# Performance work log

Measured on AMD Instinct MI355X. Metric: run time of the kernel, lower is better.

Reference implementation:

```python
import jax, jax.numpy as jnp
import numpy as np

TEMPERATURE = 0.07
EPS = 1e-8  # F.cosine_similarity eps


def setup_inputs() -> dict:
    key = jax.random.key(0)
    k1, k2, k3, k4 = jax.random.split(key, 4)
    N, D, M, C = 4096, 1024, 8192, 100
    q = jax.random.normal(k1, (N, D), dtype=jnp.float32)
    labels = jax.random.randint(k2, (N,), 0, C, dtype=jnp.int32)
    memory_logits = jax.random.normal(k3, (N, M), dtype=jnp.float32)
    memory_targets = jax.random.bernoulli(k4, 0.5, (N, M)).astype(jnp.float32)
    return {"q": q, "labels": labels, "memory_logits": memory_logits,
            "memory_targets": memory_targets}


def reference(q, labels, memory_logits, memory_targets):
    N = q.shape[0]
    # cosine similarity as normalize + GEMM (second operand detached, as in torch)
    qn = q / jnp.maximum(jnp.linalg.norm(q, axis=-1, keepdims=True), EPS)
    sims = qn @ jax.lax.stop_gradient(qn).T               # [N, N]
    src_contrast = sims / TEMPERATURE
    logits_max = jax.lax.stop_gradient(
        jnp.max(src_contrast, axis=1, keepdims=True))
    src_logits = src_contrast - logits_max                # [N, N]
    # positive-pair mask with self excluded
    src_targets = (labels[:, None] == labels[None, :]).astype(jnp.float32)
    self_mask = 1.0 - jnp.eye(N, dtype=jnp.float32)
    src_targets = src_targets * self_mask
    targets = jnp.concatenate([src_targets, memory_targets], axis=1)  # [N, N+M]
    src_exp_logits = jnp.exp(src_logits) * self_mask
    logits = jnp.concatenate([src_logits, memory_logits], axis=1)     # [N, N+M]
    denom = src_exp_logits.sum(axis=1) + jnp.exp(memory_logits).sum(axis=1)
    log_prob = logits - jnp.log(denom)[:, None]
    mean_log_prob_pos = (targets * log_prob).sum(axis=1) / targets.sum(axis=1)
    return -jnp.mean(mean_log_prob_pos)
```

## Files before the change

### kernel.cpp

```cpp
#include <hip/hip_runtime.h>
#include <hip/hip_bf16.h>
#include <math.h>

typedef unsigned short u16;
typedef __bf16 bf16x8 __attribute__((ext_vector_type(8)));
typedef float f32x4 __attribute__((ext_vector_type(4)));
typedef unsigned short u16x4 __attribute__((ext_vector_type(4)));

#define NROW 4096
#define KDIM 1024
#define MDIM 8192
#define TILE 128
#define BK 64
#define NT   (NROW / TILE)
#define NSEG (NT * 2)
#define NTRI (NT * (NT + 1) / 2)

__device__ __forceinline__ u16 f2bf(float x) {
    unsigned int u = __float_as_uint(x);
    unsigned int r = (u + 0x7fffu + ((u >> 16) & 1u)) >> 16;
    return (u16)r;
}

__device__ __forceinline__ void gload16(const u16* g, u16* l) {
    __builtin_amdgcn_global_load_lds(
        (const __attribute__((address_space(1))) void*)g,
        (__attribute__((address_space(3))) void*)l,
        16, 0, 0);
}

__global__ void k_norm_mem(const float* __restrict__ q,
                           const float* __restrict__ ml, const float* __restrict__ mt,
                           u16* __restrict__ qn, float4* __restrict__ memq) {
    const int r = blockIdx.x;
    const int t = threadIdx.x;
    const int lane = t & 63, wid = t >> 6;

    const float4* qr = (const float4*)(q + (size_t)r * KDIM);
    float4 v = qr[t];
    float ss = v.x * v.x + v.y * v.y + v.z * v.z + v.w * v.w;

    const float4* pl = (const float4*)(ml + (size_t)r * MDIM);
    const float4* pt = (const float4*)(mt + (size_t)r * MDIM);
    float S2 = 0.f, dot = 0.f, smt = 0.f;
    #pragma unroll
    for (int it = 0; it < 2; ++it) {
        const int i0 = it * 1024 + t;
        float4 l0 = pl[i0], l1 = pl[i0 + 256], l2 = pl[i0 + 512], l3 = pl[i0 + 768];
        float4 t0 = pt[i0], t1 = pt[i0 + 256], t2 = pt[i0 + 512], t3 = pt[i0 + 768];
        S2 += __expf(l0.x) + __expf(l0.y) + __expf(l0.z) + __expf(l0.w);
        S2 += __expf(l1.x) + __expf(l1.y) + __expf(l1.z) + __expf(l1.w);
        S2 += __expf(l2.x) + __expf(l2.y) + __expf(l2.z) + __expf(l2.w);
        S2 += __expf(l3.x) + __expf(l3.y) + __expf(l3.z) + __expf(l3.w);
        dot += t0.x * l0.x + t0.y * l0.y + t0.z * l0.z + t0.w * l0.w;
        dot += t1.x * l1.x + t1.y * l1.y + t1.z * l1.z + t1.w * l1.w;
        dot += t2.x * l2.x + t2.y * l2.y + t2.z * l2.z + t2.w * l2.w;
        dot += t3.x * l3.x + t3.y * l3.y + t3.z * l3.z + t3.w * l3.w;
        smt += t0.x + t0.y + t0.z + t0.w + t1.x + t1.y + t1.z + t1.w;
        smt += t2.x + t2.y + t2.z + t2.w + t3.x + t3.y + t3.z + t3.w;
    }

    #pragma unroll
    for (int d = 1; d < 64; d <<= 1) ss += __shfl_xor(ss, d);
    __shared__ float redn[4];
    if (lane == 0) redn[wid] = ss;
    __syncthreads();
    float tot = redn[0] + redn[1] + redn[2] + redn[3];
    float inv = 1.0f / fmaxf(sqrtf(tot), 1e-8f);
    u16x4 o;
    o[0] = f2bf(v.x * inv); o[1] = f2bf(v.y * inv);
    o[2] = f2bf(v.z * inv); o[3] = f2bf(v.w * inv);
    *(u16x4*)(qn + (size_t)r * KDIM + t * 4) = o;

    #pragma unroll
    for (int d = 1; d < 64; d <<= 1) {
        S2  += __shfl_xor(S2, d);
        dot += __shfl_xor(dot, d);
        smt += __shfl_xor(smt, d);
    }
    __shared__ float red[4][3];
    if (lane == 0) { red[wid][0] = S2; red[wid][1] = dot; red[wid][2] = smt; }
    __syncthreads();
    if (t == 0)
        memq[r] = make_float4(red[0][0] + red[1][0] + red[2][0] + red[3][0],
                              red[0][1] + red[1][1] + red[2][1] + red[3][1],
                              red[0][2] + red[1][2] + red[2][2] + red[3][2], 0.f);
}

__global__ void k_gemm_sym(const u16* __restrict__ qn, const int* __restrict__ labels,
                           float4* __restrict__ partials) {
    __shared__ u16 ldsA[TILE * BK];
    __shared__ u16 ldsB[TILE * BK];
    __shared__ int labR[TILE], labC[TILE];

    const int bid = blockIdx.x;
    int e = (bid & 7) * 66 + (bid >> 3);
    int rb, cb, base;
    if      (e < 36)  { rb = 0; cb = 0; base = 0;   }
    else if (e < 100) { rb = 0; cb = 1; base = 36;  }
    else if (e < 136) { rb = 1; cb = 1; base = 100; }
    else if (e < 200) { rb = 0; cb = 2; base = 136; }
    else if (e < 264) { rb = 1; cb = 2; base = 200; }
    else if (e < 300) { rb = 2; cb = 2; base = 264; }
    else if (e < 364) { rb = 0; cb = 3; base = 300; }
    else if (e < 428) { rb = 1; cb = 3; base = 364; }
    else if (e < 492) { rb = 2; cb = 3; base = 428; }
    else              { rb = 3; cb = 3; base = 492; }
    int k = e - base;
    int bi, ct;
    if (rb == cb) {
        int b2 = 0, kk = k;
        while (kk >= 8 - b2) { kk -= 8 - b2; ++b2; }
        bi = rb * 8 + b2; ct = cb * 8 + b2 + kk;
    } else {
        bi = rb * 8 + (k >> 3); ct = cb * 8 + (k & 7);
    }

    const int t = threadIdx.x;
    const int w = t >> 6, lane = t & 63;
    const int rowbase = bi * TILE, colbase = ct * TILE;

    if (t < 128) labR[t] = labels[rowbase + t];
    else labC[t - 128] = labels[colbase + (t - 128)];

    const int wr = (w >> 1) * 64, wc = (w & 1) * 64;
    const int cl = lane & 15, cg = lane >> 4;
    const int sr = lane >> 3, skb = lane & 7;

    f32x4 acc[4][4];
    #pragma unroll
    for (int i = 0; i < 4; ++i)
        #pragma unroll
        for (int j = 0; j < 4; ++j)
            acc[i][j] = {0.f, 0.f, 0.f, 0.f};

    for (int ks = 0; ks < KDIM / BK; ++ks) {
        const int k0 = ks * BK;
        #pragma unroll
        for (int it = 0; it < 4; ++it) {
            int c = w * 4 + it;
            int rr = c * 8 + sr;
            gload16(qn + (size_t)(rowbase + rr) * KDIM + k0 + skb * 8, ldsA + c * 512);
            gload16(qn + (size_t)(colbase + rr) * KDIM + k0 + skb * 8, ldsB + c * 512);
        }
        asm volatile("s_waitcnt vmcnt(0)" ::: "memory");
        __syncthreads();
        #pragma unroll
        for (int k2 = 0; k2 < 2; ++k2) {
            bf16x8 a[4], b[4];
            #pragma unroll
            for (int f = 0; f < 4; ++f) {
                a[f] = *(const bf16x8*)&ldsA[(wr + f * 16 + cl) * BK + k2 * 32 + cg * 8];
                b[f] = *(const bf16x8*)&ldsB[(wc + f * 16 + cl) * BK + k2 * 32 + cg * 8];
            }
            #pragma unroll
            for (int fm = 0; fm < 4; ++fm)
                #pragma unroll
                for (int fn = 0; fn < 4; ++fn)
                    acc[fm][fn] = __builtin_amdgcn_mfma_f32_16x16x32_bf16(
                        a[fm], b[fn], acc[fm][fn], 0, 0, 0);
        }
        __syncthreads();
    }

    const float invT = (float)(1.0 / 0.07);

    #pragma unroll
    for (int fm = 0; fm < 4; ++fm) {
        #pragma unroll
        for (int reg = 0; reg < 4; ++reg) {
            const int lr = wr + fm * 16 + cg * 4 + reg;
            const int gi = rowbase + lr;
            const int li = labR[lr];
            float c0 = acc[fm][0][reg] * invT;
            float c1 = acc[fm][1][reg] * invT;
            float c2 = acc[fm][2][reg] * invT;
            float c3 = acc[fm][3][reg] * invT;
            float m = fmaxf(fmaxf(c0, c1), fmaxf(c2, c3));
            #pragma unroll
            for (int d = 1; d < 16; d <<= 1) m = fmaxf(m, __shfl_xor(m, d));
            float se = 0.f, ps = 0.f, cnt = 0.f;
            #pragma unroll
            for (int fn = 0; fn < 4; ++fn) {
                float c = (fn == 0) ? c0 : (fn == 1) ? c1 : (fn == 2) ? c2 : c3;
                const int lc = wc + fn * 16 + cl;
                const bool self = (colbase + lc == gi);
                se += self ? 0.f : __expf(c - m);
                const bool pos = (!self) && (labC[lc] == li);
                ps += pos ? c : 0.f;
                cnt += pos ? 1.f : 0.f;
            }
            #pragma unroll
            for (int d = 1; d < 16; d <<= 1) {
                se  += __shfl_xor(se, d);
                ps  += __shfl_xor(ps, d);
                cnt += __shfl_xor(cnt, d);
            }
            if (cl == 0)
                partials[(size_t)(ct * 2 + (w & 1)) * NROW + gi] =
                    make_float4(m, se, ps, cnt);
        }
    }

    if (bi != ct) {
        #pragma unroll
        for (int fn = 0; fn < 4; ++fn) {
            const int lc = wc + fn * 16 + cl;
            const int gj = colbase + lc;
            const int lj = labC[lc];
            float m = -3.4e38f;
            #pragma unroll
            for (int fm = 0; fm < 4; ++fm)
                #pragma unroll
                for (int reg = 0; reg < 4; ++reg)
                    m = fmaxf(m, acc[fm][fn][reg] * invT);
            m = fmaxf(m, __shfl_xor(m, 16));
            m = fmaxf(m, __shfl_xor(m, 32));
            float se = 0.f, ps = 0.f, cnt = 0.f;
            #pragma unroll
            for (int fm = 0; fm < 4; ++fm) {
                #pragma unroll
                for (int reg = 0; reg < 4; ++reg) {
                    float c = acc[fm][fn][reg] * invT;
                    const int lr = wr + fm * 16 + cg * 4 + reg;
                    se += __expf(c - m);
                    const bool pos = (labR[lr] == lj);
                    ps += pos ? c : 0.f;
                    cnt += pos ? 1.f : 0.f;
                }
            }
            se += __shfl_xor(se, 16); ps += __shfl_xor(ps, 16); cnt += __shfl_xor(cnt, 16);
            se += __shfl_xor(se, 32); ps += __shfl_xor(ps, 32); cnt += __shfl_xor(cnt, 32);
            if (cg == 0)
                partials[(size_t)(bi * 2 + (w >> 1)) * NROW + gj] =
                    make_float4(m, se, ps, cnt);
        }
    }
}

__global__ void k_combine(const float4* __restrict__ partials, const float4* __restrict__ memq,
                          float* __restrict__ vals) {
    const int r = blockIdx.x * blockDim.x + threadIdx.x;
    if (r >= NROW) return;
    float M = -3.4e38f;
    #pragma unroll 8
    for (int s = 0; s < NSEG; ++s) M = fmaxf(M, partials[(size_t)s * NROW + r].x);
    float S1 = 0.f, ps = 0.f, cnt = 0.f;
    #pragma unroll 8
    for (int s = 0; s < NSEG; ++s) {
        float4 p = partials[(size_t)s * NROW + r];
        S1 += p.y * __expf(p.x - M);
        ps += p.z;
        cnt += p.w;
    }
    float4 mq = memq[r];
    float L = logf(S1 + mq.x);
    vals[r] = (ps - cnt * (M + L) + mq.y - mq.z * L) / (cnt + mq.z);
}

__global__ void k_finalize(const float* __restrict__ vals, float* __restrict__ out) {
    const int t = threadIdx.x;
    const int lane = t & 63, wid = t >> 6;
    float s = 0.f;
    for (int i = t; i < NROW; i += 256) s += vals[i];
    #pragma unroll
    for (int d = 1; d < 64; d <<= 1) s += __shfl_xor(s, d);
    __shared__ float red[4];
    if (lane == 0) red[wid] = s;
    __syncthreads();
    if (t == 0) out[0] = -(red[0] + red[1] + red[2] + red[3]) * (1.0f / (float)NROW);
}

extern "C" void kernel_launch(void* const* d_in, const int* in_sizes, int n_in,
                              void* d_out, int out_size, void* d_ws, size_t ws_size,
                              hipStream_t stream) {
    const float* q  = (const float*)d_in[0];
    const int* labels = (const int*)d_in[1];
    const float* ml = (const float*)d_in[2];
    const float* mt = (const float*)d_in[3];
    float* out = (float*)d_out;

    char* w = (char*)d_ws;
    u16* qn          = (u16*)w;
    float4* partials = (float4*)(w + 8388608);
    float4* memq     = (float4*)(w + 12582912);
    float* vals      = (float*)(w + 12648448);

    k_norm_mem<<<NROW, 256, 0, stream>>>(q, ml, mt, qn, memq);
    k_gemm_sym<<<NTRI, 256, 0, stream>>>(qn, labels, partials);
    k_combine<<<NROW / 256, 256, 0, stream>>>(partials, memq, vals);
    k_finalize<<<1, 256, 0, stream>>>(vals, out);
}
```

Before: 108.7 us.

## Overlap memory-logit reduction with symmetric GEMM in one interleaved launch

The memory-bank reduction (exp-sum, target dot and target sum over the 8192-wide rows) moves out of the normalization kernel and into the GEMM kernel. Block IDs are interleaved so that one in every eight blocks is a GEMM tile and the rest are memory-row reduction blocks. The aim is to let the bandwidth-bound streaming of memory_logits and memory_targets run at the same time as the compute-bound MFMA tiles instead of in series. The trade-off is heavier block-index arithmetic and blocks of mixed kind competing for LDS and occupancy, since reduction blocks also reserve the GEMM's LDS.

```diff
diff --git a/kernel.cpp b/kernel.cpp
--- a/kernel.cpp
+++ b/kernel.cpp
@@ -15,6 +15,7 @@
 #define NT   (NROW / TILE)
 #define NSEG (NT * 2)
 #define NTRI (NT * (NT + 1) / 2)
+#define NBLK (NROW + NTRI)
 
 __device__ __forceinline__ u16 f2bf(float x) {
     unsigned int u = __float_as_uint(x);
@@ -29,72 +30,78 @@
         16, 0, 0);
 }
 
-__global__ void k_norm_mem(const float* __restrict__ q,
-                           const float* __restrict__ ml, const float* __restrict__ mt,
-                           u16* __restrict__ qn, float4* __restrict__ memq) {
+__global__ void k_normalize(const float* __restrict__ q, u16* __restrict__ qn) {
     const int r = blockIdx.x;
     const int t = threadIdx.x;
     const int lane = t & 63, wid = t >> 6;
-
     const float4* qr = (const float4*)(q + (size_t)r * KDIM);
     float4 v = qr[t];
     float ss = v.x * v.x + v.y * v.y + v.z * v.z + v.w * v.w;
-
-    const float4* pl = (const float4*)(ml + (size_t)r * MDIM);
-    const float4* pt = (const float4*)(mt + (size_t)r * MDIM);
-    float S2 = 0.f, dot = 0.f, smt = 0.f;
-    #pragma unroll
-    for (int it = 0; it < 2; ++it) {
-        const int i0 = it * 1024 + t;
-        float4 l0 = pl[i0], l1 = pl[i0 + 256], l2 = pl[i0 + 512], l3 = pl[i0 + 768];
-        float4 t0 = pt[i0], t1 = pt[i0 + 256], t2 = pt[i0 + 512], t3 = pt[i0 + 768];
-        S2 += __expf(l0.x) + __expf(l0.y) + __expf(l0.z) + __expf(l0.w);
-        S2 += __expf(l1.x) + __expf(l1.y) + __expf(l1.z) + __expf(l1.w);
-        S2 += __expf(l2.x) + __expf(l2.y) + __expf(l2.z) + __expf(l2.w);
-        S2 += __expf(l3.x) + __expf(l3.y) + __expf(l3.z) + __expf(l3.w);
-        dot += t0.x * l0.x + t0.y * l0.y + t0.z * l0.z + t0.w * l0.w;
-        dot += t1.x * l1.x + t1.y * l1.y + t1.z * l1.z + t1.w * l1.w;
-        dot += t2.x * l2.x + t2.y * l2.y + t2.z * l2.z + t2.w * l2.w;
-        dot += t3.x * l3.x + t3.y * l3.y + t3.z * l3.z + t3.w * l3.w;
-        smt += t0.x + t0.y + t0.z + t0.w + t1.x + t1.y + t1.z + t1.w;
-        smt += t2.x + t2.y + t2.z + t2.w + t3.x + t3.y + t3.z + t3.w;
-    }
-
     #pragma unroll
     for (int d = 1; d < 64; d <<= 1) ss += __shfl_xor(ss, d);
-    __shared__ float redn[4];
-    if (lane == 0) redn[wid] = ss;
+    __shared__ float red[4];
+    if (lane == 0) red[wid] = ss;
     __syncthreads();
-    float tot = redn[0] + redn[1] + redn[2] + redn[3];
+    float tot = red[0] + red[1] + red[2] + red[3];
     float inv = 1.0f / fmaxf(sqrtf(tot), 1e-8f);
     u16x4 o;
     o[0] = f2bf(v.x * inv); o[1] = f2bf(v.y * inv);
     o[2] = f2bf(v.z * inv); o[3] = f2bf(v.w * inv);
     *(u16x4*)(qn + (size_t)r * KDIM + t * 4) = o;
-
-    #pragma unroll
-    for (int d = 1; d < 64; d <<= 1) {
-        S2  += __shfl_xor(S2, d);
-        dot += __shfl_xor(dot, d);
-        smt += __shfl_xor(smt, d);
-    }
-    __shared__ float red[4][3];
-    if (lane == 0) { red[wid][0] = S2; red[wid][1] = dot; red[wid][2] = smt; }
-    __syncthreads();
-    if (t == 0)
-        memq[r] = make_float4(red[0][0] + red[1][0] + red[2][0] + red[3][0],
-                              red[0][1] + red[1][1] + red[2][1] + red[3][1],
-                              red[0][2] + red[1][2] + red[2][2] + red[3][2], 0.f);
-}
-
-__global__ void k_gemm_sym(const u16* __restrict__ qn, const int* __restrict__ labels,
-                           float4* __restrict__ partials) {
+}
+
+__global__ void k_fused(const u16* __restrict__ qn, const int* __restrict__ labels,
+                        const float* __restrict__ ml, const float* __restrict__ mt,
+                        float4* __restrict__ partials, float4* __restrict__ memq) {
     __shared__ u16 ldsA[TILE * BK];
     __shared__ u16 ldsB[TILE * BK];
     __shared__ int labR[TILE], labC[TILE];
 
     const int bid = blockIdx.x;
-    int e = (bid & 7) * 66 + (bid >> 3);
+    const int t = threadIdx.x;
+    const int w = t >> 6, lane = t & 63;
+    const int g = bid >> 3, rr8 = bid & 7;
+    const bool is_gemm = (g < NTRI) && (rr8 == (g & 7));
+
+    if (!is_gemm) {
+        const int r = bid - (min(g, NTRI) + ((g < NTRI && rr8 > (g & 7)) ? 1 : 0));
+        const float4* pl = (const float4*)(ml + (size_t)r * MDIM);
+        const float4* pt = (const float4*)(mt + (size_t)r * MDIM);
+        float S2 = 0.f, dot = 0.f, smt = 0.f;
+        #pragma unroll
+        for (int it = 0; it < 2; ++it) {
+            const int i0 = it * 1024 + t;
+            float4 l0 = pl[i0], l1 = pl[i0 + 256], l2 = pl[i0 + 512], l3 = pl[i0 + 768];
+            float4 t0 = pt[i0], t1 = pt[i0 + 256], t2 = pt[i0 + 512], t3 = pt[i0 + 768];
+            S2 += __expf(l0.x) + __expf(l0.y) + __expf(l0.z) + __expf(l0.w);
+            S2 += __expf(l1.x) + __expf(l1.y) + __expf(l1.z) + __expf(l1.w);
+            S2 += __expf(l2.x) + __expf(l2.y) + __expf(l2.z) + __expf(l2.w);
+            S2 += __expf(l3.x) + __expf(l3.y) + __expf(l3.z) + __expf(l3.w);
+            dot += t0.x * l0.x + t0.y * l0.y + t0.z * l0.z + t0.w * l0.w;
+            dot += t1.x * l1.x + t1.y * l1.y + t1.z * l1.z + t1.w * l1.w;
+            dot += t2.x * l2.x + t2.y * l2.y + t2.z * l2.z + t2.w * l2.w;
+            dot += t3.x * l3.x + t3.y * l3.y + t3.z * l3.z + t3.w * l3.w;
+            smt += t0.x + t0.y + t0.z + t0.w + t1.x + t1.y + t1.z + t1.w;
+            smt += t2.x + t2.y + t2.z + t2.w + t3.x + t3.y + t3.z + t3.w;
+        }
+        #pragma unroll
+        for (int d = 1; d < 64; d <<= 1) {
+            S2  += __shfl_xor(S2, d);
+            dot += __shfl_xor(dot, d);
+            smt += __shfl_xor(smt, d);
+        }
+        __shared__ float red[4][3];
+        const int wid = t >> 6;
+        if (lane == 0) { red[wid][0] = S2; red[wid][1] = dot; red[wid][2] = smt; }
+        __syncthreads();
+        if (t == 0)
+            memq[r] = make_float4(red[0][0] + red[1][0] + red[2][0] + red[3][0],
+                                  red[0][1] + red[1][1] + red[2][1] + red[3][1],
+                                  red[0][2] + red[1][2] + red[2][2] + red[3][2], 0.f);
+        return;
+    }
+
+    int e = (g & 7) * 66 + (g >> 3);
     int rb, cb, base;
     if      (e < 36)  { rb = 0; cb = 0; base = 0;   }
     else if (e < 100) { rb = 0; cb = 1; base = 36;  }
@@ -116,8 +123,6 @@
         bi = rb * 8 + (k >> 3); ct = cb * 8 + (k & 7);
     }
 
-    const int t = threadIdx.x;
-    const int w = t >> 6, lane = t & 63;
     const int rowbase = bi * TILE, colbase = ct * TILE;
 
     if (t < 128) labR[t] = labels[rowbase + t];
@@ -139,9 +144,9 @@
         #pragma unroll
         for (int it = 0; it < 4; ++it) {
             int c = w * 4 + it;
-            int rr = c * 8 + sr;
-            gload16(qn + (size_t)(rowbase + rr) * KDIM + k0 + skb * 8, ldsA + c * 512);
-            gload16(qn + (size_t)(colbase + rr) * KDIM + k0 + skb * 8, ldsB + c * 512);
+            int rw = c * 8 + sr;
+            gload16(qn + (size_t)(rowbase + rw) * KDIM + k0 + skb * 8, ldsA + c * 512);
+            gload16(qn + (size_t)(colbase + rw) * KDIM + k0 + skb * 8, ldsB + c * 512);
         }
         asm volatile("s_waitcnt vmcnt(0)" ::: "memory");
         __syncthreads();
@@ -286,8 +291,8 @@
     float4* memq     = (float4*)(w + 12582912);
     float* vals      = (float*)(w + 12648448);
 
-    k_norm_mem<<<NROW, 256, 0, stream>>>(q, ml, mt, qn, memq);
-    k_gemm_sym<<<NTRI, 256, 0, stream>>>(qn, labels, partials);
+    k_normalize<<<NROW, 256, 0, stream>>>(q, qn);
+    k_fused<<<NBLK, 256, 0, stream>>>(qn, labels, ml, mt, partials, memq);
     k_combine<<<NROW / 256, 256, 0, stream>>>(partials, memq, vals);
     k_finalize<<<1, 256, 0, stream>>>(vals, out);
 }
```

Result: slower. 164.1 us (+50.9%).
